# Kernel tuning notes

Measured on AMD Instinct MI355X. Metric: run time of the kernel, lower is better.

## Reference

```python
import jax, jax.numpy as jnp
import numpy as np

B, T, S, E, H = 4, 2048, 2048, 512, 8
D = E // H  # head_dim = 64
BIFURCATION_FACTOR = 1.0


def setup_inputs() -> dict:
    key = jax.random.key(0)
    ks = jax.random.split(key, 12)
    s = 1.0 / np.sqrt(E)
    return {
        "query": jax.random.normal(ks[0], (B, T, E), jnp.float32),
        "key_": jax.random.normal(ks[1], (B, S, E), jnp.float32),
        "value": jax.random.normal(ks[2], (B, S, E), jnp.float32),
        "Wq": jax.random.uniform(ks[3], (E, E), jnp.float32, -s, s),
        "bq": jax.random.uniform(ks[4], (E,), jnp.float32, -s, s),
        "Wk": jax.random.uniform(ks[5], (E, E), jnp.float32, -s, s),
        "bk": jax.random.uniform(ks[6], (E,), jnp.float32, -s, s),
        "Wv": jax.random.uniform(ks[7], (E, E), jnp.float32, -s, s),
        "bv": jax.random.uniform(ks[8], (E,), jnp.float32, -s, s),
        "Wo": jax.random.uniform(ks[9], (E, E), jnp.float32, -s, s),
        "bo": jax.random.uniform(ks[10], (E,), jnp.float32, -s, s),
        "r": jnp.asarray(3.5, jnp.float32),
    }


def _logistic_map(x, r):
    # sigmoid-normalize then one logistic-map iteration with learned r
    xn = jax.nn.sigmoid(x)
    r_scaled = BIFURCATION_FACTOR * jax.nn.sigmoid(r) * 4.0
    return r_scaled * xn * (1.0 - xn)


def reference(query, key_, value, Wq, bq, Wk, bk, Wv, bv, Wo, bo, r):
    q = _logistic_map(query @ Wq.T + bq, r)   # [B,T,E]
    k = _logistic_map(key_ @ Wk.T + bk, r)    # [B,S,E]
    v = value @ Wv.T + bv                     # [B,S,E]

    q = q.reshape(B, T, H, D).transpose(0, 2, 1, 3)  # [B,H,T,D]
    k = k.reshape(B, S, H, D).transpose(0, 2, 1, 3)  # [B,H,S,D]
    v = v.reshape(B, S, H, D).transpose(0, 2, 1, 3)  # [B,H,S,D]

    scores = jnp.einsum('bhtd,bhsd->bhts', q, k) / jnp.sqrt(jnp.asarray(D, q.dtype))
    attn = jax.nn.softmax(scores, axis=-1)           # [B,H,T,S]
    out = jnp.einsum('bhts,bhsd->bhtd', attn, v)     # [B,H,T,D]
    out = out.transpose(0, 2, 1, 3).reshape(B, T, E)
    return out @ Wo.T + bo
```

## Files before the change

### kernel.cpp

```cpp
#include <hip/hip_runtime.h>
#include <stdint.h>

#define B_ 4
#define T_ 2048
#define S_ 2048
#define E_ 512
#define H_ 8
#define D_ 64

using bf16x8 = __attribute__((ext_vector_type(8))) short;
using bf16x4 = __attribute__((ext_vector_type(4))) short;
using f32x4  = __attribute__((ext_vector_type(4))) float;

__device__ __forceinline__ unsigned short f2bf(float f) {
  unsigned u = __float_as_uint(f);
  u += 0x7fffu + ((u >> 16) & 1u);
  return (unsigned short)(u >> 16);
}

__device__ __forceinline__ float sigmoidf_(float x) {
  return 1.0f / (1.0f + __expf(-x));
}

__device__ __forceinline__ f32x4 mfma16x16x16(bf16x4 a, bf16x4 b, f32x4 c) {
#if __has_builtin(__builtin_amdgcn_mfma_f32_16x16x16bf16_1k)
  return __builtin_amdgcn_mfma_f32_16x16x16bf16_1k(a, b, c, 0, 0, 0);
#else
  asm("v_mfma_f32_16x16x16_bf16 %0, %1, %2, %0" : "+v"(c) : "v"(a), "v"(b));
  return c;
#endif
}

__device__ __forceinline__ void gl16(const void* g, void* l) {
  __builtin_amdgcn_global_load_lds(
      (const __attribute__((address_space(1))) unsigned*)g,
      (__attribute__((address_space(3))) unsigned*)l,
      16, 0, 0);
}

__device__ __forceinline__ int swzi(int row, int ebyte) {
  return row * 64 + ((ebyte ^ ((row & 7) << 4)) >> 1);
}

__global__ __launch_bounds__(256) void cvt3_bf16(
    const float* __restrict__ a, const float* __restrict__ b, const float* __restrict__ c,
    unsigned short* __restrict__ oa, unsigned short* __restrict__ ob,
    unsigned short* __restrict__ oc, int n4) {
  int seg = blockIdx.x >> 9;
  const float* in = (seg == 0) ? a : (seg == 1) ? b : c;
  unsigned short* out = (seg == 0) ? oa : (seg == 1) ? ob : oc;
  int i = (blockIdx.x & 511) * 256 + threadIdx.x;
  for (; i < n4; i += 512 * 256) {
    float4 v = ((const float4*)in)[i];
    ushort4 o;
    o.x = f2bf(v.x); o.y = f2bf(v.y); o.z = f2bf(v.z); o.w = f2bf(v.w);
    ((ushort4*)out)[i] = o;
  }
}

__global__ __launch_bounds__(256) void cvt4_bf16(
    const float* __restrict__ a, const float* __restrict__ b,
    const float* __restrict__ c, const float* __restrict__ d,
    unsigned short* __restrict__ oa, unsigned short* __restrict__ ob,
    unsigned short* __restrict__ oc, unsigned short* __restrict__ od, int n4) {
  int seg = blockIdx.x >> 7;
  const float* in = (seg == 0) ? a : (seg == 1) ? b : (seg == 2) ? c : d;
  unsigned short* out = (seg == 0) ? oa : (seg == 1) ? ob : (seg == 2) ? oc : od;
  int i = (blockIdx.x & 127) * 256 + threadIdx.x;
  for (; i < n4; i += 128 * 256) {
    float4 v = ((const float4*)in)[i];
    ushort4 o;
    o.x = f2bf(v.x); o.y = f2bf(v.y); o.z = f2bf(v.z); o.w = f2bf(v.w);
    ((ushort4*)out)[i] = o;
  }
}

#define EPI_LH  0
#define EPI_VT  1
#define EPI_F32 2

template <int EPI>
__global__ __launch_bounds__(256) void gemm_nt(
    const unsigned short* __restrict__ A,
    const unsigned short* __restrict__ W,
    const float* __restrict__ bias,
    void* __restrict__ outp,
    const float* __restrict__ rptr,
    float oscale,
    int nTN) {
  __shared__ unsigned short As[2][128 * 64];
  __shared__ unsigned short Bs[2][64 * 64];

  int bid = ((blockIdx.x & 7) << 6) + (blockIdx.x >> 3);
  int tid = threadIdx.x;
  int lane = tid & 63, wid = tid >> 6;
  int bm = bid / nTN, bn = bid % nTN;
  int m0 = bm * 128, n0 = bn * 64;

  f32x4 acc[4][2] = {};

  int rowc = tid >> 3;
  int kswz = ((tid & 7) ^ (rowc & 7)) << 4;

  auto stage = [&](int buf, int kt) {
#pragma unroll
    for (int c = 0; c < 4; ++c) {
      const char* ga = (const char*)A + (size_t)(m0 + c * 32 + rowc) * 1024 + kt * 128 + kswz;
      gl16(ga, (char*)&As[buf][0] + c * 4096 + (wid << 10));
    }
#pragma unroll
    for (int c = 0; c < 2; ++c) {
      const char* gw = (const char*)W + (size_t)(n0 + c * 32 + rowc) * 1024 + kt * 128 + kswz;
      gl16(gw, (char*)&Bs[buf][0] + c * 4096 + (wid << 10));
    }
  };

  stage(0, 0);

  int wm = wid >> 1, wn = wid & 1;
  int fr = lane & 15, fg = lane >> 4;

  for (int kt = 0; kt < 8; ++kt) {
    __syncthreads();
    if (kt < 7) stage((kt + 1) & 1, kt + 1);
    int buf = kt & 1;
#pragma unroll
    for (int ks = 0; ks < 2; ++ks) {
      bf16x8 a[4], b[2];
#pragma unroll
      for (int mi = 0; mi < 4; ++mi)
        a[mi] = *(const bf16x8*)&As[buf][swzi(wm * 64 + mi * 16 + fr, ks * 64 + fg * 16)];
#pragma unroll
      for (int ni = 0; ni < 2; ++ni)
        b[ni] = *(const bf16x8*)&Bs[buf][swzi(wn * 32 + ni * 16 + fr, ks * 64 + fg * 16)];
#pragma unroll
      for (int mi = 0; mi < 4; ++mi)
#pragma unroll
        for (int ni = 0; ni < 2; ++ni)
          acc[mi][ni] = __builtin_amdgcn_mfma_f32_16x16x32_bf16(a[mi], b[ni], acc[mi][ni], 0, 0, 0);
    }
  }

  float rs = 0.f;
  if constexpr (EPI == EPI_LH) rs = 4.0f * sigmoidf_(rptr[0]) * oscale;

#pragma unroll
  for (int mi = 0; mi < 4; ++mi) {
#pragma unroll
    for (int ni = 0; ni < 2; ++ni) {
#pragma unroll
      for (int i = 0; i < 4; ++i) {
        int gm = m0 + wm * 64 + mi * 16 + fg * 4 + i;
        int gn = n0 + wn * 32 + ni * 16 + fr;
        float x = acc[mi][ni][i];
        if constexpr (EPI == EPI_LH) {
          x += bias[gn];
          float xn = sigmoidf_(x);
          float val = rs * xn * (1.0f - xn);
          int b = gm >> 11, t = gm & 2047, h = gn >> 6, d = gn & 63;
          ((unsigned short*)outp)[((size_t)(b * H_ + h) * T_ + t) * D_ + d] = f2bf(val);
        } else if constexpr (EPI == EPI_VT) {
          x += bias[gm];
          int h = gm >> 6, d = gm & 63, b = gn >> 11, s = gn & 2047;
          ((unsigned short*)outp)[((size_t)(b * H_ + h) * D_ + d) * S_ + s] = f2bf(x);
        } else {
          x += bias[gn];
          ((float*)outp)[(size_t)gm * E_ + gn] = x;
        }
      }
    }
  }
}

template <int CB>
__device__ __forceinline__ void tile_step(
    char* sm, int koff0, int koff1, const int (&voff)[4],
    const bf16x8 (&qa)[2][2], f32x4 (&acco)[2][4], float (&lst)[2]) {
  bf16x8 kb[4][2];
#pragma unroll
  for (int ni = 0; ni < 4; ++ni) {
    kb[ni][0] = *(const bf16x8*)(sm + CB + ni * 2048 + koff0);
    kb[ni][1] = *(const bf16x8*)(sm + CB + ni * 2048 + koff1);
  }
  f32x4 st[4][2];
#pragma unroll
  for (int ni = 0; ni < 4; ++ni)
#pragma unroll
    for (int mi = 0; mi < 2; ++mi) st[ni][mi] = f32x4{0.f, 0.f, 0.f, 0.f};

  __builtin_amdgcn_s_setprio(1);
#pragma unroll
  for (int ni = 0; ni < 4; ++ni)
#pragma unroll
    for (int mi = 0; mi < 2; ++mi)
#pragma unroll
      for (int ks = 0; ks < 2; ++ks)
        st[ni][mi] = __builtin_amdgcn_mfma_f32_16x16x32_bf16(kb[ni][ks], qa[mi][ks], st[ni][mi], 0, 0, 0);
  __builtin_amdgcn_s_setprio(0);

  union PU { unsigned u[2]; bf16x4 v; };
  bf16x4 pfr[2][4];
#pragma unroll
  for (int mi = 0; mi < 2; ++mi) {
    float sum = 0.f;
#pragma unroll
    for (int ni = 0; ni < 4; ++ni) {
      float p0 = __builtin_amdgcn_exp2f(st[ni][mi][0]);
      float p1 = __builtin_amdgcn_exp2f(st[ni][mi][1]);
      float p2 = __builtin_amdgcn_exp2f(st[ni][mi][2]);
      float p3 = __builtin_amdgcn_exp2f(st[ni][mi][3]);
      sum += (p0 + p1) + (p2 + p3);
      PU pu;
      asm("v_cvt_pk_bf16_f32 %0, %1, %2" : "=v"(pu.u[0]) : "v"(p0), "v"(p1));
      asm("v_cvt_pk_bf16_f32 %0, %1, %2" : "=v"(pu.u[1]) : "v"(p2), "v"(p3));
      pfr[mi][ni] = pu.v;
    }
    sum += __shfl_xor(sum, 16);
    sum += __shfl_xor(sum, 32);
    lst[mi] += sum;
  }

  __builtin_amdgcn_s_setprio(1);
#pragma unroll
  for (int nd = 0; nd < 4; ++nd)
#pragma unroll
    for (int ni = 0; ni < 4; ++ni) {
      bf16x4 vf = *(const bf16x4*)(sm + CB + nd * 2048 + voff[ni]);
#pragma unroll
      for (int mi = 0; mi < 2; ++mi)
        acco[mi][nd] = mfma16x16x16(vf, pfr[mi][ni], acco[mi][nd]);
    }
  __builtin_amdgcn_s_setprio(0);
}

__global__ __launch_bounds__(256) void attn_flash(
    const unsigned short* __restrict__ qp,
    const unsigned short* __restrict__ kp,
    const unsigned short* __restrict__ vtp,
    unsigned short* __restrict__ attno) {
  __shared__ __align__(16) char smem[65536];

  int tid = threadIdx.x, lane = tid & 63, wid = tid >> 6;
  int tt = blockIdx.x & 15, bh = blockIdx.x >> 4;
  const char* qh = (const char*)qp + ((size_t)bh * T_ + tt * 128) * 128;
  const char* kh = (const char*)kp + (size_t)bh * S_ * 128;
  const char* vh = (const char*)vtp + (size_t)bh * D_ * S_ * 2;

  int rowc = tid >> 3;
  int kswz = ((tid & 7) ^ (rowc & 7)) << 4;

#define STAGE_K(SB, IT) { \
    gl16(kh + (size_t)((IT) * 64 + rowc) * 128 + kswz, smem + (SB) + (wid << 10)); \
    gl16(kh + (size_t)((IT) * 64 + 32 + rowc) * 128 + kswz, smem + (SB) + 4096 + (wid << 10)); }
#define STAGE_V(SB, IT) { \
    gl16(vh + (size_t)rowc * 4096 + (IT) * 128 + kswz, smem + (SB) + 8192 + (wid << 10)); \
    gl16(vh + (size_t)(32 + rowc) * 4096 + (IT) * 128 + kswz, smem + (SB) + 12288 + (wid << 10)); }

  STAGE_K(0, 0) STAGE_V(0, 0) STAGE_K(16384, 1) STAGE_V(16384, 1)
#pragma unroll
  for (int c = 0; c < 4; ++c)
    gl16(qh + (size_t)(c * 32 + rowc) * 128 + kswz, smem + 49152 + c * 4096 + (wid << 10));

  int fr = lane & 15, fg = (lane >> 4) & 3;
  int qrb = wid * 32;
  int koff0 = fr * 128 + ((fg * 16) ^ ((fr & 7) << 4));
  int koff1 = fr * 128 + ((64 + fg * 16) ^ ((fr & 7) << 4));
  int voff[4];
#pragma unroll
  for (int ni = 0; ni < 4; ++ni)
    voff[ni] = 8192 + fr * 128 + ((ni * 32 + fg * 8) ^ ((fr & 7) << 4));

  __syncthreads();

  bf16x8 qa[2][2];
#pragma unroll
  for (int mi = 0; mi < 2; ++mi) {
    qa[mi][0] = *(const bf16x8*)(smem + 49152 + (qrb + mi * 16) * 128 + koff0);
    qa[mi][1] = *(const bf16x8*)(smem + 49152 + (qrb + mi * 16) * 128 + koff1);
  }
  __syncthreads();

  f32x4 acco[2][4] = {};
  float lst[2] = {0.f, 0.f};

  STAGE_K(32768, 2) STAGE_V(32768, 2) STAGE_K(49152, 3) STAGE_V(49152, 3)
  tile_step<0>(smem, koff0, koff1, voff, qa, acco, lst);
  tile_step<16384>(smem, koff0, koff1, voff, qa, acco, lst);

#pragma unroll 1
  for (int pp = 1; pp <= 7; ++pp) {
    int ta = pp * 4;
    __syncthreads();
    STAGE_K(0, ta) STAGE_V(0, ta) STAGE_K(16384, ta + 1) STAGE_V(16384, ta + 1)
    tile_step<32768>(smem, koff0, koff1, voff, qa, acco, lst);
    tile_step<49152>(smem, koff0, koff1, voff, qa, acco, lst);
    __syncthreads();
    STAGE_K(32768, ta + 2) STAGE_V(32768, ta + 2) STAGE_K(49152, ta + 3) STAGE_V(49152, ta + 3)
    tile_step<0>(smem, koff0, koff1, voff, qa, acco, lst);
    tile_step<16384>(smem, koff0, koff1, voff, qa, acco, lst);
  }
  __syncthreads();
  tile_step<32768>(smem, koff0, koff1, voff, qa, acco, lst);
  tile_step<49152>(smem, koff0, koff1, voff, qa, acco, lst);

  int b = bh >> 3, h = bh & 7;
#pragma unroll
  for (int mi = 0; mi < 2; ++mi) {
    float rl = 1.0f / lst[mi];
    int t = tt * 128 + qrb + mi * 16 + fr;
    unsigned short* rowp = attno + (size_t)(b * T_ + t) * E_ + h * 64;
#pragma unroll
    for (int nd = 0; nd < 4; ++nd) {
      ushort4 o;
      o.x = f2bf(acco[mi][nd][0] * rl);
      o.y = f2bf(acco[mi][nd][1] * rl);
      o.z = f2bf(acco[mi][nd][2] * rl);
      o.w = f2bf(acco[mi][nd][3] * rl);
      *(ushort4*)(rowp + nd * 16 + fg * 4) = o;
    }
  }
#undef STAGE_K
#undef STAGE_V
}

extern "C" void kernel_launch(void* const* d_in, const int* in_sizes, int n_in,
                              void* d_out, int out_size, void* d_ws, size_t ws_size,
                              hipStream_t stream) {
  const float* query = (const float*)d_in[0];
  const float* key_  = (const float*)d_in[1];
  const float* value = (const float*)d_in[2];
  const float* Wq    = (const float*)d_in[3];
  const float* bq    = (const float*)d_in[4];
  const float* Wk    = (const float*)d_in[5];
  const float* bk    = (const float*)d_in[6];
  const float* Wv    = (const float*)d_in[7];
  const float* bv    = (const float*)d_in[8];
  const float* Wo    = (const float*)d_in[9];
  const float* bo    = (const float*)d_in[10];
  const float* r     = (const float*)d_in[11];

  char* ws = (char*)d_ws;
  unsigned short* qb    = (unsigned short*)(ws + 0);
  unsigned short* kb    = (unsigned short*)(ws + 8388608);
  unsigned short* vb    = (unsigned short*)(ws + 16777216);
  unsigned short* wqb   = (unsigned short*)(ws + 25165824);
  unsigned short* wkb   = (unsigned short*)(ws + 25690112);
  unsigned short* wvb   = (unsigned short*)(ws + 26214400);
  unsigned short* wob   = (unsigned short*)(ws + 26738688);
  unsigned short* qp    = (unsigned short*)(ws + 27262976);
  unsigned short* kp    = (unsigned short*)(ws + 35651584);
  unsigned short* vtp   = (unsigned short*)(ws + 44040192);
  unsigned short* attno = (unsigned short*)(ws + 52428800);

  cvt3_bf16<<<1536, 256, 0, stream>>>(query, key_, value, qb, kb, vb, (B_ * T_ * E_) / 4);
  cvt4_bf16<<<512, 256, 0, stream>>>(Wq, Wk, Wv, Wo, wqb, wkb, wvb, wob, (E_ * E_) / 4);

  const float SCLQ = 0.125f * 1.44269504089f;

  gemm_nt<EPI_LH><<<512, 256, 0, stream>>>(qb, wqb, bq, qp, r, SCLQ, 8);
  gemm_nt<EPI_LH><<<512, 256, 0, stream>>>(kb, wkb, bk, kp, r, 1.0f, 8);
  gemm_nt<EPI_VT><<<512, 256, 0, stream>>>(wvb, vb, bv, vtp, r, 1.0f, 128);

  attn_flash<<<512, 256, 0, stream>>>(qp, kp, vtp, attno);

  gemm_nt<EPI_F32><<<512, 256, 0, stream>>>(attno, wob, bo, d_out, r, 1.0f, 8);
}
```

Baseline: 116.2 us.

## Halve attention query tile per block and double grid with XCD-aware block remap

Result: slower. 120.5 us (+3.7%).

```diff
diff --git a/kernel.cpp b/kernel.cpp
--- a/kernel.cpp
+++ b/kernel.cpp
@@ -175,50 +175,41 @@
 template <int CB>
 __device__ __forceinline__ void tile_step(
     char* sm, int koff0, int koff1, const int (&voff)[4],
-    const bf16x8 (&qa)[2][2], f32x4 (&acco)[2][4], float (&lst)[2]) {
-  bf16x8 kb[4][2];
+    bf16x8 qa0, bf16x8 qa1, f32x4 (&acco)[4], float& lst) {
+  bf16x8 kb0[4], kb1[4];
 #pragma unroll
   for (int ni = 0; ni < 4; ++ni) {
-    kb[ni][0] = *(const bf16x8*)(sm + CB + ni * 2048 + koff0);
-    kb[ni][1] = *(const bf16x8*)(sm + CB + ni * 2048 + koff1);
-  }
-  f32x4 st[4][2];
-#pragma unroll
-  for (int ni = 0; ni < 4; ++ni)
-#pragma unroll
-    for (int mi = 0; mi < 2; ++mi) st[ni][mi] = f32x4{0.f, 0.f, 0.f, 0.f};
+    kb0[ni] = *(const bf16x8*)(sm + CB + ni * 2048 + koff0);
+    kb1[ni] = *(const bf16x8*)(sm + CB + ni * 2048 + koff1);
+  }
+  f32x4 st[4] = {};
 
   __builtin_amdgcn_s_setprio(1);
 #pragma unroll
-  for (int ni = 0; ni < 4; ++ni)
-#pragma unroll
-    for (int mi = 0; mi < 2; ++mi)
-#pragma unroll
-      for (int ks = 0; ks < 2; ++ks)
-        st[ni][mi] = __builtin_amdgcn_mfma_f32_16x16x32_bf16(kb[ni][ks], qa[mi][ks], st[ni][mi], 0, 0, 0);
+  for (int ni = 0; ni < 4; ++ni) {
+    st[ni] = __builtin_amdgcn_mfma_f32_16x16x32_bf16(kb0[ni], qa0, st[ni], 0, 0, 0);
+    st[ni] = __builtin_amdgcn_mfma_f32_16x16x32_bf16(kb1[ni], qa1, st[ni], 0, 0, 0);
+  }
   __builtin_amdgcn_s_setprio(0);
 
   union PU { unsigned u[2]; bf16x4 v; };
-  bf16x4 pfr[2][4];
-#pragma unroll
-  for (int mi = 0; mi < 2; ++mi) {
-    float sum = 0.f;
-#pragma unroll
-    for (int ni = 0; ni < 4; ++ni) {
-      float p0 = __builtin_amdgcn_exp2f(st[ni][mi][0]);
-      float p1 = __builtin_amdgcn_exp2f(st[ni][mi][1]);
-      float p2 = __builtin_amdgcn_exp2f(st[ni][mi][2]);
-      float p3 = __builtin_amdgcn_exp2f(st[ni][mi][3]);
-      sum += (p0 + p1) + (p2 + p3);
-      PU pu;
-      asm("v_cvt_pk_bf16_f32 %0, %1, %2" : "=v"(pu.u[0]) : "v"(p0), "v"(p1));
-      asm("v_cvt_pk_bf16_f32 %0, %1, %2" : "=v"(pu.u[1]) : "v"(p2), "v"(p3));
-      pfr[mi][ni] = pu.v;
-    }
-    sum += __shfl_xor(sum, 16);
-    sum += __shfl_xor(sum, 32);
-    lst[mi] += sum;
-  }
+  bf16x4 pfr[4];
+  float sum = 0.f;
+#pragma unroll
+  for (int ni = 0; ni < 4; ++ni) {
+    float p0 = __builtin_amdgcn_exp2f(st[ni][0]);
+    float p1 = __builtin_amdgcn_exp2f(st[ni][1]);
+    float p2 = __builtin_amdgcn_exp2f(st[ni][2]);
+    float p3 = __builtin_amdgcn_exp2f(st[ni][3]);
+    sum += (p0 + p1) + (p2 + p3);
+    PU pu;
+    asm("v_cvt_pk_bf16_f32 %0, %1, %2" : "=v"(pu.u[0]) : "v"(p0), "v"(p1));
+    asm("v_cvt_pk_bf16_f32 %0, %1, %2" : "=v"(pu.u[1]) : "v"(p2), "v"(p3));
+    pfr[ni] = pu.v;
+  }
+  sum += __shfl_xor(sum, 16);
+  sum += __shfl_xor(sum, 32);
+  lst += sum;
 
   __builtin_amdgcn_s_setprio(1);
 #pragma unroll
@@ -226,9 +217,7 @@
 #pragma unroll
     for (int ni = 0; ni < 4; ++ni) {
       bf16x4 vf = *(const bf16x4*)(sm + CB + nd * 2048 + voff[ni]);
-#pragma unroll
-      for (int mi = 0; mi < 2; ++mi)
-        acco[mi][nd] = mfma16x16x16(vf, pfr[mi][ni], acco[mi][nd]);
+      acco[nd] = mfma16x16x16(vf, pfr[ni], acco[nd]);
     }
   __builtin_amdgcn_s_setprio(0);
 }
@@ -238,11 +227,12 @@
     const unsigned short* __restrict__ kp,
     const unsigned short* __restrict__ vtp,
     unsigned short* __restrict__ attno) {
-  __shared__ __align__(16) char smem[65536];
+  __shared__ __align__(16) char smem[32768];
 
   int tid = threadIdx.x, lane = tid & 63, wid = tid >> 6;
-  int tt = blockIdx.x & 15, bh = blockIdx.x >> 4;
-  const char* qh = (const char*)qp + ((size_t)bh * T_ + tt * 128) * 128;
+  int wgid = ((blockIdx.x & 7) << 7) + (blockIdx.x >> 3);
+  int tt = wgid & 31, bh = wgid >> 5;
+  const char* qh = (const char*)qp + ((size_t)bh * T_ + tt * 64) * 128;
   const char* kh = (const char*)kp + (size_t)bh * S_ * 128;
   const char* vh = (const char*)vtp + (size_t)bh * D_ * S_ * 2;
 
@@ -256,13 +246,12 @@
     gl16(vh + (size_t)rowc * 4096 + (IT) * 128 + kswz, smem + (SB) + 8192 + (wid << 10)); \
     gl16(vh + (size_t)(32 + rowc) * 4096 + (IT) * 128 + kswz, smem + (SB) + 12288 + (wid << 10)); }
 
-  STAGE_K(0, 0) STAGE_V(0, 0) STAGE_K(16384, 1) STAGE_V(16384, 1)
-#pragma unroll
-  for (int c = 0; c < 4; ++c)
-    gl16(qh + (size_t)(c * 32 + rowc) * 128 + kswz, smem + 49152 + c * 4096 + (wid << 10));
+  STAGE_K(0, 0) STAGE_V(0, 0)
+  gl16(qh + (size_t)rowc * 128 + kswz, smem + 16384 + (wid << 10));
+  gl16(qh + (size_t)(32 + rowc) * 128 + kswz, smem + 16384 + 4096 + (wid << 10));
 
   int fr = lane & 15, fg = (lane >> 4) & 3;
-  int qrb = wid * 32;
+  int qrb = wid * 16;
   int koff0 = fr * 128 + ((fg * 16) ^ ((fr & 7) << 4));
   int koff1 = fr * 128 + ((64 + fg * 16) ^ ((fr & 7) << 4));
   int voff[4];
@@ -272,52 +261,41 @@
 
   __syncthreads();
 
-  bf16x8 qa[2][2];
-#pragma unroll
-  for (int mi = 0; mi < 2; ++mi) {
-    qa[mi][0] = *(const bf16x8*)(smem + 49152 + (qrb + mi * 16) * 128 + koff0);
-    qa[mi][1] = *(const bf16x8*)(smem + 49152 + (qrb + mi * 16) * 128 + koff1);
-  }
+  bf16x8 qa0 = *(const bf16x8*)(smem + 16384 + qrb * 128 + koff0);
+  bf16x8 qa1 = *(const bf16x8*)(smem + 16384 + qrb * 128 + koff1);
   __syncthreads();
 
-  f32x4 acco[2][4] = {};
-  float lst[2] = {0.f, 0.f};
-
-  STAGE_K(32768, 2) STAGE_V(32768, 2) STAGE_K(49152, 3) STAGE_V(49152, 3)
-  tile_step<0>(smem, koff0, koff1, voff, qa, acco, lst);
-  tile_step<16384>(smem, koff0, koff1, voff, qa, acco, lst);
+  f32x4 acco[4] = {};
+  float lst = 0.f;
+
+  STAGE_K(16384, 1) STAGE_V(16384, 1)
+  tile_step<0>(smem, koff0, koff1, voff, qa0, qa1, acco, lst);
 
 #pragma unroll 1
-  for (int pp = 1; pp <= 7; ++pp) {
-    int ta = pp * 4;
+  for (int pp = 0; pp <= 14; ++pp) {
+    int ta = pp * 2;
     __syncthreads();
-    STAGE_K(0, ta) STAGE_V(0, ta) STAGE_K(16384, ta + 1) STAGE_V(16384, ta + 1)
-    tile_step<32768>(smem, koff0, koff1, voff, qa, acco, lst);
-    tile_step<49152>(smem, koff0, koff1, voff, qa, acco, lst);
+    STAGE_K(0, ta + 2) STAGE_V(0, ta + 2)
+    tile_step<16384>(smem, koff0, koff1, voff, qa0, qa1, acco, lst);
     __syncthreads();
-    STAGE_K(32768, ta + 2) STAGE_V(32768, ta + 2) STAGE_K(49152, ta + 3) STAGE_V(49152, ta + 3)
-    tile_step<0>(smem, koff0, koff1, voff, qa, acco, lst);
-    tile_step<16384>(smem, koff0, koff1, voff, qa, acco, lst);
+    STAGE_K(16384, ta + 3) STAGE_V(16384, ta + 3)
+    tile_step<0>(smem, koff0, koff1, voff, qa0, qa1, acco, lst);
   }
   __syncthreads();
-  tile_step<32768>(smem, koff0, koff1, voff, qa, acco, lst);
-  tile_step<49152>(smem, koff0, koff1, voff, qa, acco, lst);
+  tile_step<16384>(smem, koff0, koff1, voff, qa0, qa1, acco, lst);
 
   int b = bh >> 3, h = bh & 7;
-#pragma unroll
-  for (int mi = 0; mi < 2; ++mi) {
-    float rl = 1.0f / lst[mi];
-    int t = tt * 128 + qrb + mi * 16 + fr;
-    unsigned short* rowp = attno + (size_t)(b * T_ + t) * E_ + h * 64;
-#pragma unroll
-    for (int nd = 0; nd < 4; ++nd) {
-      ushort4 o;
-      o.x = f2bf(acco[mi][nd][0] * rl);
-      o.y = f2bf(acco[mi][nd][1] * rl);
-      o.z = f2bf(acco[mi][nd][2] * rl);
-      o.w = f2bf(acco[mi][nd][3] * rl);
-      *(ushort4*)(rowp + nd * 16 + fg * 4) = o;
-    }
+  float rl = 1.0f / lst;
+  int t = tt * 64 + qrb + fr;
+  unsigned short* rowp = attno + (size_t)(b * T_ + t) * E_ + h * 64;
+#pragma unroll
+  for (int nd = 0; nd < 4; ++nd) {
+    ushort4 o;
+    o.x = f2bf(acco[nd][0] * rl);
+    o.y = f2bf(acco[nd][1] * rl);
+    o.z = f2bf(acco[nd][2] * rl);
+    o.w = f2bf(acco[nd][3] * rl);
+    *(ushort4*)(rowp + nd * 16 + fg * 4) = o;
   }
 #undef STAGE_K
 #undef STAGE_V
@@ -361,7 +339,7 @@
   gemm_nt<EPI_LH><<<512, 256, 0, stream>>>(kb, wkb, bk, kp, r, 1.0f, 8);
   gemm_nt<EPI_VT><<<512, 256, 0, stream>>>(wvb, vb, bv, vtp, r, 1.0f, 128);
 
-  attn_flash<<<512, 256, 0, stream>>>(qp, kp, vtp, attno);
+  attn_flash<<<1024, 256, 0, stream>>>(qp, kp, vtp, attno);
 
   gemm_nt<EPI_F32><<<512, 256, 0, stream>>>(attno, wob, bo, d_out, r, 1.0f, 8);
 }
```

## Interleave two KV tiles per step and remap blocks for XCD locality

Applied to the files above, without the earlier changes.

Result: no change. 114.7 us (-1.3%).

```diff
diff --git a/kernel.cpp b/kernel.cpp
--- a/kernel.cpp
+++ b/kernel.cpp
@@ -172,48 +172,61 @@
   }
 }
 
-template <int CB>
-__device__ __forceinline__ void tile_step(
+template <int CBa, int CBb>
+__device__ __forceinline__ void tile_pair(
     char* sm, int koff0, int koff1, const int (&voff)[4],
     const bf16x8 (&qa)[2][2], f32x4 (&acco)[2][4], float (&lst)[2]) {
+  union PU { unsigned u[2]; bf16x4 v; };
+
+  bf16x8 ka[4][2];
+#pragma unroll
+  for (int ni = 0; ni < 4; ++ni) {
+    ka[ni][0] = *(const bf16x8*)(sm + CBa + ni * 2048 + koff0);
+    ka[ni][1] = *(const bf16x8*)(sm + CBa + ni * 2048 + koff1);
+  }
+  f32x4 sta[4][2] = {};
+  __builtin_amdgcn_s_setprio(1);
+#pragma unroll
+  for (int ni = 0; ni < 4; ++ni)
+#pragma unroll
+    for (int mi = 0; mi < 2; ++mi) {
+      sta[ni][mi] = __builtin_amdgcn_mfma_f32_16x16x32_bf16(ka[ni][0], qa[mi][0], sta[ni][mi], 0, 0, 0);
+      sta[ni][mi] = __builtin_amdgcn_mfma_f32_16x16x32_bf16(ka[ni][1], qa[mi][1], sta[ni][mi], 0, 0, 0);
+    }
+  __builtin_amdgcn_s_setprio(0);
+
   bf16x8 kb[4][2];
 #pragma unroll
   for (int ni = 0; ni < 4; ++ni) {
-    kb[ni][0] = *(const bf16x8*)(sm + CB + ni * 2048 + koff0);
-    kb[ni][1] = *(const bf16x8*)(sm + CB + ni * 2048 + koff1);
-  }
-  f32x4 st[4][2];
+    kb[ni][0] = *(const bf16x8*)(sm + CBb + ni * 2048 + koff0);
+    kb[ni][1] = *(const bf16x8*)(sm + CBb + ni * 2048 + koff1);
+  }
+  f32x4 stb[4][2] = {};
+  __builtin_amdgcn_s_setprio(1);
 #pragma unroll
   for (int ni = 0; ni < 4; ++ni)
 #pragma unroll
-    for (int mi = 0; mi < 2; ++mi) st[ni][mi] = f32x4{0.f, 0.f, 0.f, 0.f};
-
-  __builtin_amdgcn_s_setprio(1);
-#pragma unroll
-  for (int ni = 0; ni < 4; ++ni)
-#pragma unroll
-    for (int mi = 0; mi < 2; ++mi)
-#pragma unroll
-      for (int ks = 0; ks < 2; ++ks)
-        st[ni][mi] = __builtin_amdgcn_mfma_f32_16x16x32_bf16(kb[ni][ks], qa[mi][ks], st[ni][mi], 0, 0, 0);
+    for (int mi = 0; mi < 2; ++mi) {
+      stb[ni][mi] = __builtin_amdgcn_mfma_f32_16x16x32_bf16(kb[ni][0], qa[mi][0], stb[ni][mi], 0, 0, 0);
+      stb[ni][mi] = __builtin_amdgcn_mfma_f32_16x16x32_bf16(kb[ni][1], qa[mi][1], stb[ni][mi], 0, 0, 0);
+    }
   __builtin_amdgcn_s_setprio(0);
 
-  union PU { unsigned u[2]; bf16x4 v; };
-  bf16x4 pfr[2][4];
+  bf16x4 pfa[2][4];
 #pragma unroll
   for (int mi = 0; mi < 2; ++mi) {
     float sum = 0.f;
 #pragma unroll
     for (int ni = 0; ni < 4; ++ni) {
-      float p0 = __builtin_amdgcn_exp2f(st[ni][mi][0]);
-      float p1 = __builtin_amdgcn_exp2f(st[ni][mi][1]);
-      float p2 = __builtin_amdgcn_exp2f(st[ni][mi][2]);
-      float p3 = __builtin_amdgcn_exp2f(st[ni][mi][3]);
+      float p0 = __builtin_amdgcn_exp2f(sta[ni][mi][0]);
+      float p1 = __builtin_amdgcn_exp2f(sta[ni][mi][1]);
+      float p2 = __builtin_amdgcn_exp2f(sta[ni][mi][2]);
+      float p3 = __builtin_amdgcn_exp2f(sta[ni][mi][3]);
       sum += (p0 + p1) + (p2 + p3);
       PU pu;
       asm("v_cvt_pk_bf16_f32 %0, %1, %2" : "=v"(pu.u[0]) : "v"(p0), "v"(p1));
       asm("v_cvt_pk_bf16_f32 %0, %1, %2" : "=v"(pu.u[1]) : "v"(p2), "v"(p3));
-      pfr[mi][ni] = pu.v;
+      pfa[mi][ni] = pu.v;
     }
     sum += __shfl_xor(sum, 16);
     sum += __shfl_xor(sum, 32);
@@ -225,10 +238,43 @@
   for (int nd = 0; nd < 4; ++nd)
 #pragma unroll
     for (int ni = 0; ni < 4; ++ni) {
-      bf16x4 vf = *(const bf16x4*)(sm + CB + nd * 2048 + voff[ni]);
+      bf16x4 vf = *(const bf16x4*)(sm + CBa + nd * 2048 + voff[ni]);
 #pragma unroll
       for (int mi = 0; mi < 2; ++mi)
-        acco[mi][nd] = mfma16x16x16(vf, pfr[mi][ni], acco[mi][nd]);
+        acco[mi][nd] = mfma16x16x16(vf, pfa[mi][ni], acco[mi][nd]);
+    }
+  __builtin_amdgcn_s_setprio(0);
+
+  bf16x4 pfb[2][4];
+#pragma unroll
+  for (int mi = 0; mi < 2; ++mi) {
+    float sum = 0.f;
+#pragma unroll
+    for (int ni = 0; ni < 4; ++ni) {
+      float p0 = __builtin_amdgcn_exp2f(stb[ni][mi][0]);
+      float p1 = __builtin_amdgcn_exp2f(stb[ni][mi][1]);
+      float p2 = __builtin_amdgcn_exp2f(stb[ni][mi][2]);
+      float p3 = __builtin_amdgcn_exp2f(stb[ni][mi][3]);
+      sum += (p0 + p1) + (p2 + p3);
+      PU pu;
+      asm("v_cvt_pk_bf16_f32 %0, %1, %2" : "=v"(pu.u[0]) : "v"(p0), "v"(p1));
+      asm("v_cvt_pk_bf16_f32 %0, %1, %2" : "=v"(pu.u[1]) : "v"(p2), "v"(p3));
+      pfb[mi][ni] = pu.v;
+    }
+    sum += __shfl_xor(sum, 16);
+    sum += __shfl_xor(sum, 32);
+    lst[mi] += sum;
+  }
+
+  __builtin_amdgcn_s_setprio(1);
+#pragma unroll
+  for (int nd = 0; nd < 4; ++nd)
+#pragma unroll
+    for (int ni = 0; ni < 4; ++ni) {
+      bf16x4 vf = *(const bf16x4*)(sm + CBb + nd * 2048 + voff[ni]);
+#pragma unroll
+      for (int mi = 0; mi < 2; ++mi)
+        acco[mi][nd] = mfma16x16x16(vf, pfb[mi][ni], acco[mi][nd]);
     }
   __builtin_amdgcn_s_setprio(0);
 }
@@ -241,7 +287,8 @@
   __shared__ __align__(16) char smem[65536];
 
   int tid = threadIdx.x, lane = tid & 63, wid = tid >> 6;
-  int tt = blockIdx.x & 15, bh = blockIdx.x >> 4;
+  int wgid = ((blockIdx.x & 7) << 6) + (blockIdx.x >> 3);
+  int tt = wgid & 15, bh = wgid >> 4;
   const char* qh = (const char*)qp + ((size_t)bh * T_ + tt * 128) * 128;
   const char* kh = (const char*)kp + (size_t)bh * S_ * 128;
   const char* vh = (const char*)vtp + (size_t)bh * D_ * S_ * 2;
@@ -284,24 +331,20 @@
   float lst[2] = {0.f, 0.f};
 
   STAGE_K(32768, 2) STAGE_V(32768, 2) STAGE_K(49152, 3) STAGE_V(49152, 3)
-  tile_step<0>(smem, koff0, koff1, voff, qa, acco, lst);
-  tile_step<16384>(smem, koff0, koff1, voff, qa, acco, lst);
+  tile_pair<0, 16384>(smem, koff0, koff1, voff, qa, acco, lst);
 
 #pragma unroll 1
   for (int pp = 1; pp <= 7; ++pp) {
     int ta = pp * 4;
     __syncthreads();
     STAGE_K(0, ta) STAGE_V(0, ta) STAGE_K(16384, ta + 1) STAGE_V(16384, ta + 1)
-    tile_step<32768>(smem, koff0, koff1, voff, qa, acco, lst);
-    tile_step<49152>(smem, koff0, koff1, voff, qa, acco, lst);
+    tile_pair<32768, 49152>(smem, koff0, koff1, voff, qa, acco, lst);
     __syncthreads();
     STAGE_K(32768, ta + 2) STAGE_V(32768, ta + 2) STAGE_K(49152, ta + 3) STAGE_V(49152, ta + 3)
-    tile_step<0>(smem, koff0, koff1, voff, qa, acco, lst);
-    tile_step<16384>(smem, koff0, koff1, voff, qa, acco, lst);
+    tile_pair<0, 16384>(smem, koff0, koff1, voff, qa, acco, lst);
   }
   __syncthreads();
-  tile_step<32768>(smem, koff0, koff1, voff, qa, acco, lst);
-  tile_step<49152>(smem, koff0, koff1, voff, qa, acco, lst);
+  tile_pair<32768, 49152>(smem, koff0, koff1, voff, qa, acco, lst);
 
   int b = bh >> 3, h = bh & 7;
 #pragma unroll
```
